# Kernel optimization log

Hardware: AMD Instinct MI355X
Metric: run time of the kernel (lower is better)

The kernel has to match this reference:

```python
import jax, jax.numpy as jnp
import numpy as np

EPS = 1e-15
MAX_ATANH = 1.0 - 1e-5
V = 2097152   # total nodes (B*N*L flattened)
E = 8388608   # edges, ~avg degree 4 (temporal + parent/child)
ATT = 16
MAXD = 512    # mixer embedding table size
# curvature c = 1.0 (registered buffer, constant)


def _mobius_add(a, b):
    # Poincare ball Mobius addition, c = 1
    a2 = jnp.sum(a * a, -1, keepdims=True)
    b2 = jnp.sum(b * b, -1, keepdims=True)
    ab = jnp.sum(a * b, -1, keepdims=True)
    num = (1.0 + 2.0 * ab + b2) * a + (1.0 - a2) * b
    den = 1.0 + 2.0 * ab + a2 * b2
    return num / jnp.maximum(den, EPS)


def _log_map_x(x, y):
    # log_x(y): tangent vector at x pointing to y (c = 1)
    sub = _mobius_add(-x, y)
    n = jnp.maximum(jnp.linalg.norm(sub, axis=-1, keepdims=True), EPS)
    lam = 2.0 / jnp.maximum(1.0 - jnp.sum(x * x, -1, keepdims=True), EPS)
    return (2.0 / lam) * jnp.arctanh(jnp.minimum(n, MAX_ATANH)) * (sub / n)


def _exp_map_x(x, v):
    # exp_x(v) (c = 1)
    n = jnp.maximum(jnp.linalg.norm(v, axis=-1, keepdims=True), EPS)
    lam = 2.0 / jnp.maximum(1.0 - jnp.sum(x * x, -1, keepdims=True), EPS)
    return _mobius_add(x, jnp.tanh(0.5 * lam * n) * (v / n))


def setup_inputs() -> dict:
    key = jax.random.key(0)
    ks = jax.random.split(key, 8)
    # node embeddings strictly inside the unit ball: exp0 of a small tangent vec
    v0 = 0.5 * jax.random.normal(ks[0], (V, 2), jnp.float32)
    n0 = jnp.maximum(jnp.linalg.norm(v0, axis=-1, keepdims=True), EPS)
    x = jnp.tanh(n0) * v0 / n0
    edge_index = jax.random.randint(ks[1], (2, E), 0, V)
    depth = jax.random.randint(ks[2], (V,), 0, MAXD)
    W1 = jax.random.normal(ks[3], (2, ATT), jnp.float32) / jnp.sqrt(2.0)
    b1 = 0.1 * jax.random.normal(ks[4], (ATT,), jnp.float32)
    W2 = jax.random.normal(ks[5], (ATT, 1), jnp.float32) / jnp.sqrt(float(ATT))
    eta = jnp.float32(1.0)
    depth_scale = 1.0 + 0.01 * jax.random.normal(ks[6], (MAXD,), jnp.float32)
    depth_theta = 0.01 * jax.random.normal(ks[7], (MAXD,), jnp.float32)
    return {"x": x, "W1": W1, "b1": b1, "W2": W2, "eta": eta,
            "depth_scale": depth_scale, "depth_theta": depth_theta,
            "edge_index": edge_index, "depth": depth}


def reference(x, W1, b1, W2, eta, depth_scale, depth_theta, edge_index, depth):
    row, col = edge_index[0], edge_index[1]
    xi = x[row]                      # [E,2] gather target endpoints
    xj = x[col]                      # [E,2] gather source endpoints
    v_ij = _log_map_x(xi, xj)        # [E,2] hyperbolic log-map
    # small per-edge MLP scorer: Linear(2,16) -> GELU(exact) -> Linear(16,1)
    h = jax.nn.gelu(v_ij @ W1 + b1, approximate=False)
    scores = (h @ W2)[:, 0]          # [E]
    # segment softmax over target node (row)
    mx = jax.ops.segment_max(scores, row, num_segments=V)
    e = jnp.exp(scores - mx[row])
    den = jax.ops.segment_sum(e, row, num_segments=V)
    alpha = e / jnp.maximum(den[row], EPS)
    # scatter-add aggregate in tangent space
    m = jax.ops.segment_sum(alpha[:, None] * v_ij, row, num_segments=V)  # [V,2]
    # depth-gated mixer: per-node scale + 2D rotation
    d = jnp.minimum(depth, MAXD - 1)
    k = depth_scale[d][:, None]
    ang = depth_theta[d]
    ca, sa = jnp.cos(ang), jnp.sin(ang)
    m = k * jnp.stack([ca * m[:, 0] - sa * m[:, 1],
                       sa * m[:, 0] + ca * m[:, 1]], axis=-1)
    # exp-map update
    return _exp_map_x(x, eta * m)
```

## Files before the change

### kernel.cpp

```cpp
#include <hip/hip_runtime.h>
#include <hip/hip_fp16.h>
#include <math.h>

#define EPSF 1e-15f
#define MAX_ATANH (1.0f - 1e-5f)
#define ATT 16

#define LOG_NPB 11
#define NPB (1 << LOG_NPB)
#define MAXB 1024
#define NBLK 512

#define TDIM 512
#define TSPAN 12.5f
#define TSTEP (TSPAN / (float)(TDIM - 1))
#define TSCALE ((float)(TDIM - 1) / TSPAN)
#define TOFF (6.25f * TSCALE)

#define NRESCUE 0.97f

__device__ __forceinline__ float fast_atanh(float z) {
    return 0.5f * __logf(__fdividef(1.0f + z, 1.0f - z));
}
__device__ __forceinline__ float fast_tanh(float z) {
    return 1.0f - __fdividef(2.0f, __expf(2.0f * z) + 1.0f);
}
__device__ __forceinline__ float gelu_exact(float u) {
    return 0.5f * u * (1.0f + erff(u * 0.70710678118654752f));
}

__global__ void __launch_bounds__(256) x2h_kernel(const float4* __restrict__ x4,
                                                  __half2* __restrict__ xh, int Vhalf) {
    const int i = blockIdx.x * 256 + threadIdx.x;
    if (i >= Vhalf) return;
    const float4 v = x4[i];
    xh[2 * i]     = __floats2half2_rn(v.x, v.y);
    xh[2 * i + 1] = __floats2half2_rn(v.z, v.w);
}

__global__ void __launch_bounds__(256) build_table_kernel(
        const float* __restrict__ W1, const float* __restrict__ b1,
        const float* __restrict__ W2, float2* __restrict__ tab) {
    const int idx = blockIdx.x * 256 + threadIdx.x;
    if (idx >= TDIM * TDIM) return;
    const int iy = idx >> 9;
    const int ix = idx & (TDIM - 1);
    const float vy  = fmaf((float)iy, TSTEP, -6.25f);
    const float vx0 = fmaf((float)ix, TSTEP, -6.25f);
    const float vx1 = fmaf((float)min(ix + 1, TDIM - 1), TSTEP, -6.25f);
    float s0 = 0.0f, s1 = 0.0f;
    #pragma unroll
    for (int k = 0; k < ATT; ++k) {
        const float w1x = W1[k], w1y = W1[ATT + k], bb = b1[k], w2 = W2[k];
        s0 = fmaf(gelu_exact(fmaf(vx0, w1x, fmaf(vy, w1y, bb))), w2, s0);
        s1 = fmaf(gelu_exact(fmaf(vx1, w1x, fmaf(vy, w1y, bb))), w2, s1);
    }
    tab[idx] = make_float2(s0, s1);
}

__global__ void __launch_bounds__(256) hist_kernel(const int* __restrict__ row,
                                                   int E, int B,
                                                   unsigned* __restrict__ counts ) {
    __shared__ unsigned h[MAXB];
    for (int i = threadIdx.x; i < B; i += 256) h[i] = 0u;
    __syncthreads();
    const int T = gridDim.x * 256;
    const int nv = E >> 2;
    const int4* row4 = (const int4*)row;
    for (int i = blockIdx.x * 256 + threadIdx.x; i < nv; i += T) {
        const int4 r = row4[i];
        atomicAdd(&h[((unsigned)r.x) >> LOG_NPB], 1u);
        atomicAdd(&h[((unsigned)r.y) >> LOG_NPB], 1u);
        atomicAdd(&h[((unsigned)r.z) >> LOG_NPB], 1u);
        atomicAdd(&h[((unsigned)r.w) >> LOG_NPB], 1u);
    }
    for (int e = (nv << 2) + blockIdx.x * 256 + threadIdx.x; e < E; e += T)
        atomicAdd(&h[((unsigned)row[e]) >> LOG_NPB], 1u);
    __syncthreads();
    for (int i = threadIdx.x; i < B; i += 256)
        counts[(size_t)i * gridDim.x + blockIdx.x] = h[i];
}

__global__ void __launch_bounds__(256) scan_blocks_kernel(const unsigned* __restrict__ counts,
                                                          unsigned* __restrict__ within,
                                                          unsigned* __restrict__ totals) {
    const int b = blockIdx.x;
    const unsigned* src = counts + (size_t)b * NBLK;
    unsigned* dst = within + (size_t)b * NBLK;
    __shared__ unsigned s[256];
    unsigned v0, v1;
    {
        const uint2 v = ((const uint2*)src)[threadIdx.x];
        v0 = v.x; v1 = v.y;
    }
    s[threadIdx.x] = v0 + v1;
    __syncthreads();
    for (int off = 1; off < 256; off <<= 1) {
        unsigned t = (threadIdx.x >= off) ? s[threadIdx.x - off] : 0u;
        __syncthreads();
        s[threadIdx.x] += t;
        __syncthreads();
    }
    unsigned base = (threadIdx.x > 0) ? s[threadIdx.x - 1] : 0u;
    uint2 o;
    o.x = base; o.y = base + v0;
    ((uint2*)dst)[threadIdx.x] = o;
    if (threadIdx.x == 255) totals[b] = s[255];
}

__global__ void __launch_bounds__(256) scan_totals_kernel(const unsigned* __restrict__ totals,
                                                          unsigned* __restrict__ base, int B) {
    __shared__ unsigned s[256];
    unsigned vals[8];
    const int i0 = threadIdx.x * 8;
    unsigned sum = 0u;
    #pragma unroll
    for (int k = 0; k < 8; ++k) {
        vals[k] = (i0 + k < B) ? totals[i0 + k] : 0u;
        sum += vals[k];
    }
    s[threadIdx.x] = sum;
    __syncthreads();
    for (int off = 1; off < 256; off <<= 1) {
        unsigned t = (threadIdx.x >= off) ? s[threadIdx.x - off] : 0u;
        __syncthreads();
        s[threadIdx.x] += t;
        __syncthreads();
    }
    unsigned b0 = (threadIdx.x > 0) ? s[threadIdx.x - 1] : 0u;
    #pragma unroll
    for (int k = 0; k < 8; ++k) {
        if (i0 + k < B) base[i0 + k] = b0;
        b0 += vals[k];
    }
    if (threadIdx.x == 255) base[B] = s[255];
}

__global__ void __launch_bounds__(256) scatter_kernel(const int* __restrict__ row,
                                                      const int* __restrict__ col,
                                                      int E, int B,
                                                      const unsigned* __restrict__ base,
                                                      const unsigned* __restrict__ within,
                                                      unsigned* __restrict__ payload) {
    __shared__ unsigned cur[MAXB];
    const int nblk = gridDim.x;
    for (int i = threadIdx.x; i < B; i += 256)
        cur[i] = base[i] + within[(size_t)i * nblk + blockIdx.x];
    __syncthreads();
    const int T = nblk * 256;
    const int nv = E >> 2;
    const int4* row4 = (const int4*)row;
    const int4* col4 = (const int4*)col;
    for (int i = blockIdx.x * 256 + threadIdx.x; i < nv; i += T) {
        const int4 r = row4[i];
        const int4 c = col4[i];
        {
            const unsigned rr = (unsigned)r.x;
            const unsigned pos = atomicAdd(&cur[rr >> LOG_NPB], 1u);
            payload[pos] = ((rr & (NPB - 1)) << 21) | (unsigned)c.x;
        }
        {
            const unsigned rr = (unsigned)r.y;
            const unsigned pos = atomicAdd(&cur[rr >> LOG_NPB], 1u);
            payload[pos] = ((rr & (NPB - 1)) << 21) | (unsigned)c.y;
        }
        {
            const unsigned rr = (unsigned)r.z;
            const unsigned pos = atomicAdd(&cur[rr >> LOG_NPB], 1u);
            payload[pos] = ((rr & (NPB - 1)) << 21) | (unsigned)c.z;
        }
        {
            const unsigned rr = (unsigned)r.w;
            const unsigned pos = atomicAdd(&cur[rr >> LOG_NPB], 1u);
            payload[pos] = ((rr & (NPB - 1)) << 21) | (unsigned)c.w;
        }
    }
    for (int e = (nv << 2) + blockIdx.x * 256 + threadIdx.x; e < E; e += T) {
        const unsigned rr = (unsigned)row[e];
        const unsigned pos = atomicAdd(&cur[rr >> LOG_NPB], 1u);
        payload[pos] = ((rr & (NPB - 1)) << 21) | (unsigned)col[e];
    }
}

__device__ __forceinline__ void sub_norm(float2 xi, float2 xj,
                                         float& subx, float& suby, float& n) {
    const float ax = -xi.x, ay = -xi.y;
    const float bx = xj.x,  by = xj.y;
    const float a2 = ax * ax + ay * ay;
    const float b2 = bx * bx + by * by;
    const float ab = ax * bx + ay * by;
    const float ca = 1.0f + 2.0f * ab + b2;
    const float cb = 1.0f - a2;
    const float dn = fmaxf(1.0f + 2.0f * ab + a2 * b2, EPSF);
    const float rdn = __fdividef(1.0f, dn);
    subx = (ca * ax + cb * bx) * rdn;
    suby = (ca * ay + cb * by) * rdn;
    n = fmaxf(sqrtf(subx * subx + suby * suby), EPSF);
}

__device__ __forceinline__ void edge_single(unsigned p, int nodeBase,
        const float2* __restrict__ x, const __half2* __restrict__ xh,
        const float2* __restrict__ tab,
        float* sden, float* smx, float* smy) {
    const unsigned lrow = p >> 21;
    const unsigned c = p & 0x1FFFFFu;
    float2 xj = __half22float2(xh[c]);
    const float2 xi = x[nodeBase + (int)lrow];

    float subx, suby, n;
    sub_norm(xi, xj, subx, suby, n);
    if (n > NRESCUE) {
        xj = x[c];
        sub_norm(xi, xj, subx, suby, n);
    }

    const float M = fmaxf(1.0f - (xi.x * xi.x + xi.y * xi.y), EPSF);
    const float scl = M * fast_atanh(fminf(n, MAX_ATANH)) * __fdividef(1.0f, n);
    const float vx = scl * subx;
    const float vy = scl * suby;

    float tx = fmaf(vx, TSCALE, TOFF);
    float ty = fmaf(vy, TSCALE, TOFF);
    tx = fminf(fmaxf(tx, 0.0f), 510.999f);
    ty = fminf(fmaxf(ty, 0.0f), 510.999f);
    const int ix = (int)tx;
    const int iy = (int)ty;
    const float fx = tx - (float)ix;
    const float fy = ty - (float)iy;
    const int baseIdx = (iy << 9) + ix;
    const float2 r0 = tab[baseIdx];
    const float2 r1 = tab[baseIdx + TDIM];
    const float s0 = fmaf(fx, r0.y - r0.x, r0.x);
    const float s1 = fmaf(fx, r1.y - r1.x, r1.x);
    const float s  = fmaf(fy, s1 - s0, s0);

    const float ee = __expf(s);
    atomicAdd(&sden[lrow], ee);
    atomicAdd(&smx[lrow], ee * vx);
    atomicAdd(&smy[lrow], ee * vy);
}

__global__ void __launch_bounds__(512, 8) bucket_reduce_kernel(
        const float2* __restrict__ x,
        const __half2* __restrict__ xh,
        const float2* __restrict__ tab,
        const unsigned* __restrict__ base,
        const unsigned* __restrict__ payload,
        const int* __restrict__ depth,
        const float* __restrict__ depth_scale,
        const float* __restrict__ depth_theta,
        const float* __restrict__ eta_p,
        float2* __restrict__ out, int V) {
    __shared__ float  sden[NPB];
    __shared__ float  smx[NPB];
    __shared__ float  smy[NPB];
    const int b = blockIdx.x;
    const int nodeBase = b << LOG_NPB;
    for (int i = threadIdx.x; i < NPB; i += 512) {
        sden[i] = 0.f; smx[i] = 0.f; smy[i] = 0.f;
    }
    __syncthreads();

    const unsigned e0 = base[b], e1 = base[b + 1];
    for (unsigned e = e0 + threadIdx.x; e < e1; e += 512)
        edge_single(payload[e], nodeBase, x, xh, tab, sden, smx, smy);
    __syncthreads();

    const float eta = eta_p[0];
    for (int i = threadIdx.x; i < NPB; i += 512) {
        const int v = nodeBase + i;
        if (v >= V) break;
        const float rdv = __fdividef(1.0f, fmaxf(sden[i], EPSF));
        const float mx = smx[i] * rdv;
        const float my = smy[i] * rdv;

        const int d = min(depth[v], 511);
        const float k   = depth_scale[d];
        const float ang = depth_theta[d];
        const float cs = __cosf(ang), sn = __sinf(ang);
        const float m0 = eta * (k * (cs * mx - sn * my));
        const float m1 = eta * (k * (sn * mx + cs * my));

        const float2 xi = x[v];

        const float n = fmaxf(sqrtf(m0 * m0 + m1 * m1), EPSF);
        const float M = fmaxf(1.0f - (xi.x * xi.x + xi.y * xi.y), EPSF);
        const float t = fast_tanh(__fdividef(n, M));
        const float tn = t * __fdividef(1.0f, n);
        const float bx = tn * m0;
        const float by = tn * m1;

        const float a2 = xi.x * xi.x + xi.y * xi.y;
        const float b2 = bx * bx + by * by;
        const float ab = xi.x * bx + xi.y * by;
        const float ca = 1.0f + 2.0f * ab + b2;
        const float cb = 1.0f - a2;
        const float dn = fmaxf(1.0f + 2.0f * ab + a2 * b2, EPSF);
        const float rdn = __fdividef(1.0f, dn);

        out[v] = make_float2((ca * xi.x + cb * bx) * rdn,
                             (ca * xi.y + cb * by) * rdn);
    }
}

extern "C" void kernel_launch(void* const* d_in, const int* in_sizes, int n_in,
                              void* d_out, int out_size, void* d_ws, size_t ws_size,
                              hipStream_t stream) {
    const float2* x          = (const float2*)d_in[0];
    const float*  W1         = (const float*)d_in[1];
    const float*  b1         = (const float*)d_in[2];
    const float*  W2         = (const float*)d_in[3];
    const float*  eta        = (const float*)d_in[4];
    const float*  dscale     = (const float*)d_in[5];
    const float*  dtheta     = (const float*)d_in[6];
    const int*    edge_index = (const int*)d_in[7];
    const int*    depth      = (const int*)d_in[8];

    const int V = in_sizes[0] / 2;
    const int E = in_sizes[7] / 2;
    const int B = (V + NPB - 1) >> LOG_NPB;

    const int* row = edge_index;
    const int* col = edge_index + E;

    unsigned* payload = (unsigned*)d_ws;
    unsigned* counts  = payload + E;
    unsigned* within  = counts + (size_t)B * NBLK;
    unsigned* totals  = within + (size_t)B * NBLK;
    unsigned* base    = totals + B;
    __half2*  xh      = (__half2*)(base + B + 1);
    float2*   tab     = (float2*)within;

    hist_kernel<<<NBLK, 256, 0, stream>>>(row, E, B, counts);
    scan_blocks_kernel<<<B, 256, 0, stream>>>(counts, within, totals);
    scan_totals_kernel<<<1, 256, 0, stream>>>(totals, base, B);
    scatter_kernel<<<NBLK, 256, 0, stream>>>(row, col, E, B, base, within, payload);
    x2h_kernel<<<(V / 2 + 255) / 256, 256, 0, stream>>>((const float4*)x, xh, V / 2);
    build_table_kernel<<<(TDIM * TDIM) / 256, 256, 0, stream>>>(W1, b1, W2, tab);
    bucket_reduce_kernel<<<B, 512, 0, stream>>>(x, xh, tab, base, payload,
                                                depth, dscale, dtheta, eta,
                                                (float2*)d_out, V);
}
```

Measured before the change: 280.4 us.

## Embed half-precision source coordinates into scatter payload to avoid random gathers

The scatter kernel now gathers the fp16 source-node coordinates by column index and stores them next to the packed row/col word, so each payload entry becomes 8 bytes. The bucket reduce kernel reads xj directly from the payload instead of doing a random gather into xh. The conversion kernel is moved ahead of the scatter so the half data exists when it is read. This moves the random gather into the scatter pass, which already streams col, and doubles payload write/read traffic in exchange for removing a dependent random load in the reduce loop.

```diff
diff --git a/kernel.cpp b/kernel.cpp
--- a/kernel.cpp
+++ b/kernel.cpp
@@ -138,10 +138,11 @@
 
 __global__ void __launch_bounds__(256) scatter_kernel(const int* __restrict__ row,
                                                       const int* __restrict__ col,
+                                                      const unsigned* __restrict__ xhbits,
                                                       int E, int B,
                                                       const unsigned* __restrict__ base,
                                                       const unsigned* __restrict__ within,
-                                                      unsigned* __restrict__ payload) {
+                                                      uint2* __restrict__ payload) {
     __shared__ unsigned cur[MAXB];
     const int nblk = gridDim.x;
     for (int i = threadIdx.x; i < B; i += 256)
@@ -154,31 +155,37 @@
     for (int i = blockIdx.x * 256 + threadIdx.x; i < nv; i += T) {
         const int4 r = row4[i];
         const int4 c = col4[i];
+        const unsigned j0 = xhbits[(unsigned)c.x];
+        const unsigned j1 = xhbits[(unsigned)c.y];
+        const unsigned j2 = xhbits[(unsigned)c.z];
+        const unsigned j3 = xhbits[(unsigned)c.w];
         {
             const unsigned rr = (unsigned)r.x;
             const unsigned pos = atomicAdd(&cur[rr >> LOG_NPB], 1u);
-            payload[pos] = ((rr & (NPB - 1)) << 21) | (unsigned)c.x;
+            payload[pos] = make_uint2(((rr & (NPB - 1)) << 21) | (unsigned)c.x, j0);
         }
         {
             const unsigned rr = (unsigned)r.y;
             const unsigned pos = atomicAdd(&cur[rr >> LOG_NPB], 1u);
-            payload[pos] = ((rr & (NPB - 1)) << 21) | (unsigned)c.y;
+            payload[pos] = make_uint2(((rr & (NPB - 1)) << 21) | (unsigned)c.y, j1);
         }
         {
             const unsigned rr = (unsigned)r.z;
             const unsigned pos = atomicAdd(&cur[rr >> LOG_NPB], 1u);
-            payload[pos] = ((rr & (NPB - 1)) << 21) | (unsigned)c.z;
+            payload[pos] = make_uint2(((rr & (NPB - 1)) << 21) | (unsigned)c.z, j2);
         }
         {
             const unsigned rr = (unsigned)r.w;
             const unsigned pos = atomicAdd(&cur[rr >> LOG_NPB], 1u);
-            payload[pos] = ((rr & (NPB - 1)) << 21) | (unsigned)c.w;
+            payload[pos] = make_uint2(((rr & (NPB - 1)) << 21) | (unsigned)c.w, j3);
         }
     }
     for (int e = (nv << 2) + blockIdx.x * 256 + threadIdx.x; e < E; e += T) {
         const unsigned rr = (unsigned)row[e];
+        const unsigned cc = (unsigned)col[e];
+        const unsigned jb = xhbits[cc];
         const unsigned pos = atomicAdd(&cur[rr >> LOG_NPB], 1u);
-        payload[pos] = ((rr & (NPB - 1)) << 21) | (unsigned)col[e];
+        payload[pos] = make_uint2(((rr & (NPB - 1)) << 21) | cc, jb);
     }
 }
 
@@ -198,13 +205,14 @@
     n = fmaxf(sqrtf(subx * subx + suby * suby), EPSF);
 }
 
-__device__ __forceinline__ void edge_single(unsigned p, int nodeBase,
-        const float2* __restrict__ x, const __half2* __restrict__ xh,
-        const float2* __restrict__ tab,
+__device__ __forceinline__ void edge_single(uint2 pw, int nodeBase,
+        const float2* __restrict__ x, const float2* __restrict__ tab,
         float* sden, float* smx, float* smy) {
+    const unsigned p = pw.x;
     const unsigned lrow = p >> 21;
     const unsigned c = p & 0x1FFFFFu;
-    float2 xj = __half22float2(xh[c]);
+    const __half2 hj = *reinterpret_cast<const __half2*>(&pw.y);
+    float2 xj = __half22float2(hj);
     const float2 xi = x[nodeBase + (int)lrow];
 
     float subx, suby, n;
@@ -242,10 +250,9 @@
 
 __global__ void __launch_bounds__(512, 8) bucket_reduce_kernel(
         const float2* __restrict__ x,
-        const __half2* __restrict__ xh,
         const float2* __restrict__ tab,
         const unsigned* __restrict__ base,
-        const unsigned* __restrict__ payload,
+        const uint2* __restrict__ payload,
         const int* __restrict__ depth,
         const float* __restrict__ depth_scale,
         const float* __restrict__ depth_theta,
@@ -263,7 +270,7 @@
 
     const unsigned e0 = base[b], e1 = base[b + 1];
     for (unsigned e = e0 + threadIdx.x; e < e1; e += 512)
-        edge_single(payload[e], nodeBase, x, xh, tab, sden, smx, smy);
+        edge_single(payload[e], nodeBase, x, tab, sden, smx, smy);
     __syncthreads();
 
     const float eta = eta_p[0];
@@ -323,21 +330,23 @@
     const int* row = edge_index;
     const int* col = edge_index + E;
 
-    unsigned* payload = (unsigned*)d_ws;
-    unsigned* counts  = payload + E;
+    unsigned* payw    = (unsigned*)d_ws;
+    unsigned* counts  = payw + 2 * (size_t)E;
     unsigned* within  = counts + (size_t)B * NBLK;
     unsigned* totals  = within + (size_t)B * NBLK;
     unsigned* base    = totals + B;
-    __half2*  xh      = (__half2*)(base + B + 1);
+    unsigned* xhbits  = base + B + 1;
+    uint2*    payload = (uint2*)payw;
+    __half2*  xh      = (__half2*)xhbits;
     float2*   tab     = (float2*)within;
 
     hist_kernel<<<NBLK, 256, 0, stream>>>(row, E, B, counts);
     scan_blocks_kernel<<<B, 256, 0, stream>>>(counts, within, totals);
     scan_totals_kernel<<<1, 256, 0, stream>>>(totals, base, B);
-    scatter_kernel<<<NBLK, 256, 0, stream>>>(row, col, E, B, base, within, payload);
     x2h_kernel<<<(V / 2 + 255) / 256, 256, 0, stream>>>((const float4*)x, xh, V / 2);
+    scatter_kernel<<<NBLK, 256, 0, stream>>>(row, col, xhbits, E, B, base, within, payload);
     build_table_kernel<<<(TDIM * TDIM) / 256, 256, 0, stream>>>(W1, b1, W2, tab);
-    bucket_reduce_kernel<<<B, 512, 0, stream>>>(x, xh, tab, base, payload,
+    bucket_reduce_kernel<<<B, 512, 0, stream>>>(x, tab, base, payload,
                                                 depth, dscale, dtheta, eta,
                                                 (float2*)d_out, V);
 }
```

Result: slower. 371.9 us (+32.7%).
